# Kernel tuning notes

Hardware: AMD Instinct MI355X
Metric: run time of the kernel (lower is better)

Reference implementation:

```python
import jax, jax.numpy as jnp
import numpy as np

N_CRYST = 64
ATOMS_PER = 32
N = N_CRYST * ATOMS_PER          # 2048 atoms
NBR = 20                         # max_neighbors
E = N * NBR                      # 40960 edges
C = 128                          # sphere_channels(_reduce)
HID = 256                        # hidden_channels
NB = 128                         # num_basis_functions
NLAYER = 8                       # num_interactions
LMAX = 6
K = 1 + 3 * LMAX                 # SH coeffs with mmax=1 -> 19
MAXZ = 100                       # MAX_ATOMIC_NUM
ZDIM = 256
CUT = 8.0
FOUR_PI = 4.0 * np.pi


def sph_harm_m01(d):
    """Real spherical harmonics Y_l^m, l<=LMAX, m in {-1,0,1}. d: [E,3] unit vecs -> [E,K]."""
    x, y, ct = d[:, 0], d[:, 1], d[:, 2]
    rho = jnp.sqrt(x * x + y * y) + 1e-12   # sin(theta)
    cph, sph = x / rho, y / rho
    # Legendre P_l(ct)
    P0 = [jnp.ones_like(ct), ct]
    for l in range(2, LMAX + 1):
        P0.append(((2 * l - 1) * ct * P0[l - 1] - (l - 1) * P0[l - 2]) / l)
    # Associated Legendre P_l^1(ct)
    P1 = {1: -rho, 2: -3.0 * ct * rho}
    for l in range(3, LMAX + 1):
        P1[l] = ((2 * l - 1) * ct * P1[l - 1] - l * P1[l - 2]) / (l - 1)
    Ys = [jnp.full_like(ct, float(np.sqrt(1.0 / FOUR_PI)))]
    for l in range(1, LMAX + 1):
        K0 = float(np.sqrt((2 * l + 1) / FOUR_PI))
        K1 = float(np.sqrt(2.0 * (2 * l + 1) / FOUR_PI / (l * (l + 1))))
        Ys += [K1 * P1[l] * sph, K0 * P0[l], K1 * P1[l] * cph]  # m=-1,0,+1
    return jnp.stack(Ys, axis=-1)


def lattice_from_params(lengths, angles):
    """lengths,angles(deg): [B,3] -> lattice row-vectors [B,3,3]."""
    a, b, c = lengths[:, 0], lengths[:, 1], lengths[:, 2]
    rad = angles * (np.pi / 180.0)
    ca, cb, cg = jnp.cos(rad[:, 0]), jnp.cos(rad[:, 1]), jnp.cos(rad[:, 2])
    sg = jnp.sin(rad[:, 2])
    z0 = jnp.zeros_like(a)
    v3y = (ca - cb * cg) / sg
    v3z = jnp.sqrt(jnp.clip(1.0 - cb * cb - v3y * v3y, 1e-8))
    l1 = jnp.stack([a, z0, z0], -1)
    l2 = jnp.stack([b * cg, b * sg, z0], -1)
    l3 = jnp.stack([c * cb, c * v3y, c * v3z], -1)
    return jnp.stack([l1, l2, l3], axis=1)


def setup_inputs() -> dict:
    key = jax.random.key(0)
    ks = jax.random.split(key, 16)
    z = jax.random.normal(ks[0], (N_CRYST, ZDIM), jnp.float32)
    frac = jax.random.uniform(ks[1], (N, 3), jnp.float32)
    atom_types = jax.random.randint(ks[2], (N,), 1, MAXZ + 1)
    num_atoms = jnp.full((N_CRYST,), ATOMS_PER, jnp.int32)
    lengths = 4.0 + 4.0 * jax.random.uniform(ks[3], (N_CRYST, 3), jnp.float32)
    angles = 80.0 + 20.0 * jax.random.uniform(ks[4], (N_CRYST, 3), jnp.float32)
    batch = jnp.arange(N) // ATOMS_PER
    # NBR incoming edges per atom, sources restricted to the same crystal
    dst = jnp.repeat(jnp.arange(N), NBR)
    src_local = jax.random.randint(ks[5], (E,), 0, ATOMS_PER)
    src = (dst // ATOMS_PER) * ATOMS_PER + src_local
    edge_index = jnp.stack([src, dst], axis=0)
    sc = lambda k, sh, fan: jax.random.normal(k, sh, jnp.float32) / np.sqrt(fan)
    params = dict(
        emb=sc(ks[6], (MAXZ + 1, C), 1.0),
        zproj=sc(ks[7], (ZDIM, C), ZDIM),
        Wd=sc(ks[8], (NLAYER, NB, HID), NB),
        W1=sc(ks[9], (NLAYER, C, HID), C),
        W2=sc(ks[10], (NLAYER, HID, C), HID),
        Wa=sc(ks[11], (C, MAXZ), C),
        ba=jnp.zeros((MAXZ,), jnp.float32),
        wf=sc(ks[12], (C,), C),
    )
    return dict(z=z, pred_frac_coords=frac, pred_atom_types=atom_types,
                num_atoms=num_atoms, lengths=lengths, angles=angles,
                batch=batch, edge_index=edge_index, **params)


def reference(z, pred_frac_coords, pred_atom_types, num_atoms, lengths, angles,
              batch, edge_index, emb, zproj, Wd, W1, W2, Wa, ba, wf):
    lat = lattice_from_params(lengths, angles)                 # [B,3,3]
    pos = jnp.einsum('ni,nij->nj', pred_frac_coords, lat[batch])  # [N,3]
    src, dst = edge_index[0], edge_index[1]
    vec = pos[src] - pos[dst]                                  # [E,3]
    dist = jnp.linalg.norm(vec, axis=-1) + 1e-8
    dirn = vec / dist[:, None]
    offsets = jnp.linspace(0.0, CUT, NB)
    width = offsets[1] - offsets[0]
    rbf = jnp.exp(-0.5 * ((dist[:, None] - offsets) / width) ** 2)  # [E,NB]
    Y = sph_harm_m01(dirn)                                     # [E,K]
    # node SH features, l=0 initialized from atom embedding + latent
    x = jnp.zeros((N, K, C), pred_frac_coords.dtype)
    x = x.at[:, 0, :].set(emb[pred_atom_types] + (z @ zproj)[batch])
    for l in range(NLAYER):
        s = jnp.einsum('ek,ekc->ec', Y, x[src])                # project along edge frame
        h = jax.nn.silu(s @ W1[l] + rbf @ Wd[l])               # [E,HID]
        m = h @ W2[l]                                          # [E,C]
        agg = jax.ops.segment_sum(Y[:, :, None] * m[:, None, :], dst, num_segments=N)
        x = x + agg / NBR
    h_node = x[:, 0, :]                                        # [N,C]
    atom_logits = h_node @ Wa + ba                             # [N,MAXZ]
    fscal = (h_node[src] - h_node[dst]) @ wf                   # [E]
    coord_diff = jax.ops.segment_sum(fscal[:, None] * dirn, dst, num_segments=N)
    return coord_diff, atom_logits
```

## Files before the change

### kernel.cpp

```cpp
#include <hip/hip_runtime.h>
#include <hip/hip_bf16.h>

#define N_CRYST 64
#define ATOMS_PER 32
#define NN 2048
#define NBRS 20
#define EE 40960
#define CC 128
#define HIDDIM 256
#define NBASIS 128
#define NLAYERS 8
#define LMAXV 6
#define KK 19
#define MAXZV 100
#define ZDIMV 256
#define FOUR_PI_F 12.566370614359172f

typedef unsigned short ushort_t;
typedef __attribute__((ext_vector_type(8))) short short8;
typedef __attribute__((ext_vector_type(4))) float floatx4;

__device__ __forceinline__ ushort_t f2us(float f) {
    union { float f; unsigned u; } x;
    x.f = f;
    unsigned r = (x.u + 0x7fffu + ((x.u >> 16) & 1u)) >> 16;
    return (ushort_t)r;
}
__device__ __forceinline__ float us2f(unsigned u) {
    return __uint_as_float(u << 16);
}

__global__ void k_geom(const float* __restrict__ frac, const float* __restrict__ lengths,
                       const float* __restrict__ angles, const int* __restrict__ ei,
                       const float* __restrict__ z, const float* __restrict__ zproj,
                       float* __restrict__ dist, float* __restrict__ dirn,
                       float* __restrict__ Yv, int* __restrict__ trp,
                       int* __restrict__ tloc, float* __restrict__ zc) {
    const int cr = blockIdx.x;
    const int t = threadIdx.x;
    __shared__ float posL[32][3];
    __shared__ int cnt[8][32], base[8][32];

    if (t < 32) {
        int n = cr * 32 + t;
        float la = lengths[cr * 3 + 0];
        float lb = lengths[cr * 3 + 1];
        float lc = lengths[cr * 3 + 2];
        const float D2R = 0.017453292519943295f;
        float aa = angles[cr * 3 + 0] * D2R;
        float ab = angles[cr * 3 + 1] * D2R;
        float ag = angles[cr * 3 + 2] * D2R;
        float ca = cosf(aa), cb = cosf(ab), cg = cosf(ag), sg = sinf(ag);
        float v3y = (ca - cb * cg) / sg;
        float v3z = sqrtf(fmaxf(1.0f - cb * cb - v3y * v3y, 1e-8f));
        float f0 = frac[n * 3 + 0];
        float f1 = frac[n * 3 + 1];
        float f2 = frac[n * 3 + 2];
        posL[t][0] = f0 * la + f1 * (lb * cg) + f2 * (lc * cb);
        posL[t][1] = f1 * (lb * sg) + f2 * (lc * v3y);
        posL[t][2] = f2 * (lc * v3z);
    }
    cnt[t >> 5][t & 31] = 0;
    __syncthreads();

    for (int j = t; j < 640; j += 256) {
        int e = cr * 640 + j;
        int s = ei[e] - cr * 32, d = ei[EE + e] - cr * 32;
        float vx = posL[s][0] - posL[d][0];
        float vy = posL[s][1] - posL[d][1];
        float vz = posL[s][2] - posL[d][2];
        float dd = sqrtf(vx * vx + vy * vy + vz * vz) + 1e-8f;
        float ix = vx / dd, iy = vy / dd, iz = vz / dd;
        dist[e] = dd;
        dirn[e * 3 + 0] = ix;
        dirn[e * 3 + 1] = iy;
        dirn[e * 3 + 2] = iz;

        float ct = iz;
        float rho = sqrtf(ix * ix + iy * iy) + 1e-12f;
        float cph = ix / rho, sph = iy / rho;
        float P0[LMAXV + 1], P1[LMAXV + 1];
        P0[0] = 1.0f;
        P0[1] = ct;
        #pragma unroll
        for (int l = 2; l <= LMAXV; l++)
            P0[l] = ((2 * l - 1) * ct * P0[l - 1] - (l - 1) * P0[l - 2]) / (float)l;
        P1[0] = 0.0f;
        P1[1] = -rho;
        P1[2] = -3.0f * ct * rho;
        #pragma unroll
        for (int l = 3; l <= LMAXV; l++)
            P1[l] = ((2 * l - 1) * ct * P1[l - 1] - l * P1[l - 2]) / (float)(l - 1);

        float* Ye = Yv + (size_t)e * KK;
        Ye[0] = 0.28209479177387814f;
        #pragma unroll
        for (int l = 1; l <= LMAXV; l++) {
            float K0 = sqrtf((2 * l + 1) / FOUR_PI_F);
            float K1 = sqrtf(2.0f * (2 * l + 1) / (FOUR_PI_F * l * (l + 1)));
            Ye[3 * l - 2] = K1 * P1[l] * sph;
            Ye[3 * l - 1] = K0 * P0[l];
            Ye[3 * l]     = K1 * P1[l] * cph;
        }
        atomicAdd(&cnt[j / 80][s], 1);
    }
    __syncthreads();

    if (t < 8) {
        int run = 0;
        for (int a = 0; a < 32; a++) {
            base[t][a] = run;
            trp[(cr * 8 + t) * 33 + a] = run;
            run += cnt[t][a];
        }
        trp[(cr * 8 + t) * 33 + 32] = run;
    }
    __syncthreads();
    cnt[t >> 5][t & 31] = 0;
    __syncthreads();
    for (int j = t; j < 640; j += 256) {
        int e = cr * 640 + j;
        int s = ei[e] - cr * 32;
        int tt = j / 80;
        int slot = base[tt][s] + atomicAdd(&cnt[tt][s], 1);
        tloc[(cr * 8 + tt) * 80 + slot] = j - tt * 80;
    }

    if (t < CC) {
        float acc = 0.f;
        const float* zb = z + (size_t)cr * ZDIMV;
        for (int d = 0; d < ZDIMV; d++) acc += zb[d] * zproj[d * CC + t];
        zc[cr * CC + t] = acc;
    }
}

#define WT_BLKS 3072
#define RBF_BLKS 2560
#define XI_BLKS 4864
__global__ void k_prep(const float* __restrict__ W1, const float* __restrict__ Wd,
                       const float* __restrict__ W2,
                       ushort_t* __restrict__ WT1, ushort_t* __restrict__ WT2,
                       const float* __restrict__ dist, ushort_t* __restrict__ Abf,
                       const int* __restrict__ atype, const int* __restrict__ batch,
                       const float* __restrict__ emb, const float* __restrict__ zc,
                       ushort_t* __restrict__ xbf) {
    const int bid = blockIdx.x;
    const int t = threadIdx.x;
    if (bid < WT_BLKS) {
        int idx = bid * 256 + t;
        const int n1 = NLAYERS * HIDDIM * 256;
        if (idx < n1) {
            int l = idx >> 16;
            int r = idx & 65535;
            int n = r >> 8, k = r & 255;
            float v = (k < 128) ? W1[((size_t)l * CC + k) * HIDDIM + n]
                                : Wd[((size_t)l * NBASIS + (k - 128)) * HIDDIM + n];
            WT1[idx] = f2us(v);
        } else {
            int j = idx - n1;
            int l = j >> 15;
            int r = j & 32767;
            int n = r >> 8, k = r & 255;
            WT2[j] = f2us(W2[((size_t)l * HIDDIM + k) * CC + n]);
        }
    } else if (bid < WT_BLKS + RBF_BLKS) {
        int idx = (bid - WT_BLKS) * 256 + t;
        int e = idx >> 4, j8 = (idx & 15) * 8;
        const float width = 8.0f / 127.0f;
        const float invw = 127.0f / 8.0f;
        float dd = dist[e];
        short8 v;
        #pragma unroll
        for (int jj = 0; jj < 8; jj++) {
            float x = (dd - (float)(j8 + jj) * width) * invw;
            ((ushort_t*)&v)[jj] = f2us(__expf(-0.5f * x * x));
        }
        *(short8*)&Abf[(size_t)e * 256 + 128 + j8] = v;
    } else {
        int idx4 = (bid - WT_BLKS - RBF_BLKS) * 256 + t;
        int basei = idx4 * 4;
        if (basei >= NN * KK * CC) return;
        int n = basei / (KK * CC);
        int r = basei - n * (KK * CC);
        ushort_t v4[4];
        #pragma unroll
        for (int j = 0; j < 4; j++) {
            int rr = r + j;
            float v = 0.f;
            if (rr < CC) v = emb[atype[n] * CC + rr] + zc[batch[n] * CC + rr];
            v4[j] = f2us(v);
        }
        *(uint2*)&xbf[basei] = *(uint2*)v4;
    }
}

__global__ __launch_bounds__(512, 2) void k_layer(const int* __restrict__ trp,
                                                  const int* __restrict__ tloc,
                                                  const float* __restrict__ Yv,
                                                  const ushort_t* __restrict__ Abf,
                                                  const ushort_t* __restrict__ WT1,
                                                  const ushort_t* __restrict__ WT2,
                                                  const ushort_t* __restrict__ xbfin,
                                                  ushort_t* __restrict__ xbfout) {
    __shared__ char smraw[47360];
    ushort_t* As  = (ushort_t*)smraw;
    ushort_t* Hs  = (ushort_t*)smraw;
    ushort_t* Ms  = (ushort_t*)smraw;
    float*   Ylds = (float*)(smraw + 40960);

    const int t = threadIdx.x;
    const int bid = ((blockIdx.x & 7) << 6) | (blockIdx.x >> 3);
    const int w = t >> 6, lane = t & 63;
    const int quad = lane >> 4, lrow = lane & 15;
    const int e0 = bid * 80;
    const int cr = bid >> 3;

    const float* Yb = Yv + (size_t)e0 * KK;
    #pragma unroll
    for (int j = 0; j < 3; j++) {
        int i = t + j * 512;
        if (i < 80 * KK) Ylds[(i / KK) * 20 + (i % KK)] = Yb[i];
    }
    if (t < 80) Ylds[t * 20 + 19] = 0.f;
    __syncthreads();

    short8 arg[3];
    #pragma unroll
    for (int i = 0; i < 3; i++) {
        int idx = i * 512 + t;
        if (idx < 1280) {
            int r = idx >> 4, g16 = idx & 15;
            arg[i] = *(const short8*)(Abf + (size_t)(e0 + r) * 256 + 128 + g16 * 8);
        }
    }

    const int c2 = lane * 2;
    const int sgrp = lane >> 2;
    const int soff = (lane & 3) * 2;
    #pragma unroll 1
    for (int a8 = 0; a8 < 4; a8++) {
        const int a = w * 4 + a8;
        const int i0 = trp[bid * 33 + a];
        const int i1 = trp[bid * 33 + a + 1];
        if (i0 == i1) continue;
        const ushort_t* xsrc = xbfin + (size_t)(cr * 32 + a) * (KK * CC) + c2;
        float2 xr[KK];
        #pragma unroll
        for (int k = 0; k < KK; k++) {
            unsigned u = *(const unsigned*)(xsrc + k * CC);
            xr[k] = make_float2(us2f(u & 0xffffu), us2f(u >> 16));
        }
        for (int i = i0; i < i1; i++) {
            const int r = tloc[bid * 80 + i];
            const float* yp = Ylds + r * 20;
            float ax = 0.f, ay = 0.f;
            #pragma unroll
            for (int k = 0; k < KK; k++) {
                float y = yp[k];
                ax += y * xr[k].x;
                ay += y * xr[k].y;
            }
            unsigned pk = (unsigned)f2us(ax) | (((unsigned)f2us(ay)) << 16);
            *(unsigned*)&As[r * 256 + ((sgrp ^ (r & 7)) << 3) + soff] = pk;
        }
    }

    #pragma unroll
    for (int i = 0; i < 3; i++) {
        int idx = i * 512 + t;
        if (idx < 1280) {
            int r = idx >> 4, g = 16 + (idx & 15);
            *(short8*)&As[r * 256 + ((g ^ (r & 7)) << 3)] = arg[i];
        }
    }

    const ushort_t* W1w = WT1 + (size_t)(w * 32) * 256;
    short8 bp0[2], bp1[2];
    #pragma unroll
    for (int ni = 0; ni < 2; ni++) {
        bp0[ni] = *(const short8*)(W1w + (size_t)(ni * 16 + lrow) * 256 + quad * 8);
        bp1[ni] = *(const short8*)(W1w + (size_t)(ni * 16 + lrow) * 256 + 32 + quad * 8);
    }
    __syncthreads();

    floatx4 acc[5][2];
    #pragma unroll
    for (int mi = 0; mi < 5; mi++)
        #pragma unroll
        for (int ni = 0; ni < 2; ni++) acc[mi][ni] = (floatx4){0.f, 0.f, 0.f, 0.f};

    #pragma unroll
    for (int s8 = 0; s8 < 8; s8++) {
        short8 bcur[2];
        if (s8 & 1) {
            #pragma unroll
            for (int ni = 0; ni < 2; ni++) bcur[ni] = bp1[ni];
            if (s8 < 6) {
                const int kn = (s8 + 2) * 32 + quad * 8;
                #pragma unroll
                for (int ni = 0; ni < 2; ni++)
                    bp1[ni] = *(const short8*)(W1w + (size_t)(ni * 16 + lrow) * 256 + kn);
            }
        } else {
            #pragma unroll
            for (int ni = 0; ni < 2; ni++) bcur[ni] = bp0[ni];
            if (s8 < 6) {
                const int kn = (s8 + 2) * 32 + quad * 8;
                #pragma unroll
                for (int ni = 0; ni < 2; ni++)
                    bp0[ni] = *(const short8*)(W1w + (size_t)(ni * 16 + lrow) * 256 + kn);
            }
        }
        const int grp = s8 * 4 + quad;
        short8 af[5];
        #pragma unroll
        for (int mi = 0; mi < 5; mi++) {
            const int r = mi * 16 + lrow;
            af[mi] = *(const short8*)&As[r * 256 + ((grp ^ (r & 7)) << 3)];
        }
        __builtin_amdgcn_s_setprio(1);
        #pragma unroll
        for (int ni = 0; ni < 2; ni++)
            #pragma unroll
            for (int mi = 0; mi < 5; mi++)
                acc[mi][ni] = __builtin_amdgcn_mfma_f32_16x16x32_bf16(
                    af[mi], bcur[ni], acc[mi][ni], 0, 0, 0);
        __builtin_amdgcn_s_setprio(0);
    }

    const ushort_t* W2w = WT2 + (size_t)(w * 16) * 256;
    short8 bq0, bq1;
    bq0 = *(const short8*)(W2w + (size_t)lrow * 256 + quad * 8);
    bq1 = *(const short8*)(W2w + (size_t)lrow * 256 + 32 + quad * 8);
    __syncthreads();

    #pragma unroll
    for (int mi = 0; mi < 5; mi++) {
        const int row = mi * 16 + quad * 4;
        #pragma unroll
        for (int ni = 0; ni < 2; ni++) {
            const int col = w * 32 + ni * 16 + lrow;
            #pragma unroll
            for (int r = 0; r < 4; r++) {
                float v = acc[mi][ni][r];
                v = v * __builtin_amdgcn_rcpf(1.0f + __expf(-v));
                const int rr = row + r;
                Hs[rr * 256 + ((((col >> 3) ^ (rr & 7)) << 3) | (col & 7))] = f2us(v);
            }
        }
    }
    __syncthreads();

    floatx4 macc[5];
    #pragma unroll
    for (int mi = 0; mi < 5; mi++) macc[mi] = (floatx4){0.f, 0.f, 0.f, 0.f};

    #pragma unroll
    for (int s8 = 0; s8 < 8; s8++) {
        short8 bcur;
        if (s8 & 1) {
            bcur = bq1;
            if (s8 < 6) {
                const int kn = (s8 + 2) * 32 + quad * 8;
                bq1 = *(const short8*)(W2w + (size_t)lrow * 256 + kn);
            }
        } else {
            bcur = bq0;
            if (s8 < 6) {
                const int kn = (s8 + 2) * 32 + quad * 8;
                bq0 = *(const short8*)(W2w + (size_t)lrow * 256 + kn);
            }
        }
        const int grp = s8 * 4 + quad;
        short8 af[5];
        #pragma unroll
        for (int mi = 0; mi < 5; mi++) {
            const int r = mi * 16 + lrow;
            af[mi] = *(const short8*)&Hs[r * 256 + ((grp ^ (r & 7)) << 3)];
        }
        __builtin_amdgcn_s_setprio(1);
        #pragma unroll
        for (int mi = 0; mi < 5; mi++)
            macc[mi] = __builtin_amdgcn_mfma_f32_16x16x32_bf16(
                af[mi], bcur, macc[mi], 0, 0, 0);
        __builtin_amdgcn_s_setprio(0);
    }
    __syncthreads();

    #pragma unroll
    for (int mi = 0; mi < 5; mi++) {
        const int row = mi * 16 + quad * 4;
        const int col = w * 16 + lrow;
        #pragma unroll
        for (int r = 0; r < 4; r++)
            Ms[(row + r) * 132 + col] = f2us(macc[mi][r]);
    }
    __syncthreads();

    const int node = t >> 7;
    const int cq = t & 127;
    const int ng = bid * 4 + node;
    const ushort_t* xbi = xbfin + (size_t)ng * (KK * CC) + cq;
    ushort_t* xbo = xbfout + (size_t)ng * (KK * CC) + cq;

    float xold[KK];
    #pragma unroll
    for (int k = 0; k < KK; k++) xold[k] = us2f((unsigned)xbi[k * CC]);

    float xacc[KK];
    #pragma unroll
    for (int k = 0; k < KK; k++) xacc[k] = 0.f;

    #pragma unroll 4
    for (int e = 0; e < NBRS; e++) {
        const int eg = node * NBRS + e;
        const float m0 = us2f((unsigned)Ms[eg * 132 + cq]);
        const float* yp = Ylds + eg * 20;
        #pragma unroll
        for (int kq = 0; kq < 5; kq++) {
            float4 y = *(const float4*)(yp + kq * 4);
            const int k = kq * 4;
            xacc[k + 0] += y.x * m0;
            xacc[k + 1] += y.y * m0;
            xacc[k + 2] += y.z * m0;
            if (kq < 4) xacc[k + 3] += y.w * m0;
        }
    }
    const float s = 1.0f / (float)NBRS;
    #pragma unroll
    for (int k = 0; k < KK; k++) {
        float nv = xold[k] + xacc[k] * s;
        xbo[k * CC] = f2us(nv);
    }
}

#define COORD_BLKS 512
__global__ void k_head(const int* __restrict__ ei, const ushort_t* __restrict__ xbf,
                       const float* __restrict__ wf, const float* __restrict__ dirn,
                       const float* __restrict__ Wa, const float* __restrict__ ba,
                       float* __restrict__ out) {
    const int bid = blockIdx.x;
    const int t = threadIdx.x;
    if (bid < COORD_BLKS) {
        __shared__ float fs[4][NBRS];
        __shared__ float wsh[CC];
        const int g = t >> 6, lane = t & 63;
        const int n = bid * 4 + g;
        if (t < CC) wsh[t] = wf[t];
        __syncthreads();
        if (lane < NBRS) {
            int e = n * NBRS + lane;
            int sidx = ei[e];
            const ushort_t* xs = xbf + (size_t)sidx * (KK * CC);
            const ushort_t* xd = xbf + (size_t)n * (KK * CC);
            float acc = 0.0f;
            for (int c = 0; c < CC; c++)
                acc += (us2f((unsigned)xs[c]) - us2f((unsigned)xd[c])) * wsh[c];
            fs[g][lane] = acc;
        }
        __syncthreads();
        if (lane < 3) {
            float acc = 0.0f;
            #pragma unroll
            for (int j = 0; j < NBRS; j++)
                acc += fs[g][j] * dirn[(size_t)(n * NBRS + j) * 3 + lane];
            out[n * 3 + lane] = acc;
        }
    } else {
        int idx = (bid - COORD_BLKS) * 256 + t;
        if (idx >= NN * MAXZV) return;
        int n = idx / MAXZV, a = idx - n * MAXZV;
        float acc = ba[a];
        const ushort_t* hn = xbf + (size_t)n * (KK * CC);
        for (int c = 0; c < CC; c++) acc += us2f((unsigned)hn[c]) * Wa[c * MAXZV + a];
        out[NN * 3 + idx] = acc;
    }
}

extern "C" void kernel_launch(void* const* d_in, const int* in_sizes, int n_in,
                              void* d_out, int out_size, void* d_ws, size_t ws_size,
                              hipStream_t stream) {
    (void)in_sizes; (void)n_in; (void)out_size; (void)ws_size;
    const float* z       = (const float*)d_in[0];
    const float* frac    = (const float*)d_in[1];
    const int*   atype   = (const int*)d_in[2];
    const float* lengths = (const float*)d_in[4];
    const float* angles  = (const float*)d_in[5];
    const int*   batch   = (const int*)d_in[6];
    const int*   ei      = (const int*)d_in[7];
    const float* emb     = (const float*)d_in[8];
    const float* zproj   = (const float*)d_in[9];
    const float* Wd      = (const float*)d_in[10];
    const float* W1      = (const float*)d_in[11];
    const float* W2      = (const float*)d_in[12];
    const float* Wa      = (const float*)d_in[13];
    const float* ba      = (const float*)d_in[14];
    const float* wf      = (const float*)d_in[15];
    float* out = (float*)d_out;

    float* ws = (float*)d_ws;
    float* dist = ws; ws += EE;
    float* dirn = ws; ws += EE * 3;
    float* Yv   = ws; ws += (size_t)EE * KK + 4;
    float* zc   = ws; ws += N_CRYST * CC;
    ushort_t* xbfA = (ushort_t*)ws; ws += (size_t)NN * KK * CC / 2;
    ushort_t* xbfB = (ushort_t*)ws; ws += (size_t)NN * KK * CC / 2;
    int* trp  = (int*)ws;
    int* tloc = trp + 512 * 33;
    ushort_t* Abf  = (ushort_t*)(tloc + 512 * 80);
    ushort_t* WT1  = Abf + (size_t)EE * 256;
    ushort_t* WT2  = WT1 + (size_t)NLAYERS * 256 * 256;

    k_geom<<<N_CRYST, 256, 0, stream>>>(frac, lengths, angles, ei, z, zproj,
                                        dist, dirn, Yv, trp, tloc, zc);
    k_prep<<<WT_BLKS + RBF_BLKS + XI_BLKS, 256, 0, stream>>>(W1, Wd, W2, WT1, WT2,
                                                             dist, Abf, atype, batch,
                                                             emb, zc, xbfA);

    for (int l = 0; l < NLAYERS; l++) {
        const ushort_t* xbi = (l & 1) ? xbfB : xbfA;
        ushort_t*       xbo = (l & 1) ? xbfA : xbfB;
        k_layer<<<512, 512, 0, stream>>>(trp, tloc, Yv, Abf,
                                         WT1 + (size_t)l * 256 * 256,
                                         WT2 + (size_t)l * CC * HIDDIM,
                                         xbi, xbo);
    }

    k_head<<<COORD_BLKS + (NN * MAXZV) / 256, 256, 0, stream>>>(ei, xbfA, wf, dirn,
                                                                Wa, ba, out);
}
```

Before: 411.5 us.

## Fuse next-layer edge projection into layer epilogue and compact RBF buffer

After each layer updates the node features, the same threads now project the fresh node state onto the outgoing edges of that node (via a new per-crystal CSR of source edges) and write the next layer's edge input s in bf16. The following layer then loads s directly into shared memory instead of gathering 19xC node features per edge and reducing them. The RBF buffer is also shrunk to 128 columns per edge. This trades the gather-and-reduce prologue for extra global traffic: scattered Y reads from global memory and an additional E×C bf16 write and read per layer.

```diff
diff --git a/kernel.cpp b/kernel.cpp
--- a/kernel.cpp
+++ b/kernel.cpp
@@ -35,11 +35,13 @@
                        const float* __restrict__ z, const float* __restrict__ zproj,
                        float* __restrict__ dist, float* __restrict__ dirn,
                        float* __restrict__ Yv, int* __restrict__ trp,
-                       int* __restrict__ tloc, float* __restrict__ zc) {
+                       int* __restrict__ tloc, int* __restrict__ crow,
+                       int* __restrict__ corig, float* __restrict__ zc) {
     const int cr = blockIdx.x;
     const int t = threadIdx.x;
     __shared__ float posL[32][3];
     __shared__ int cnt[8][32], base[8][32];
+    __shared__ int ccnt[32], cbs[32];
 
     if (t < 32) {
         int n = cr * 32 + t;
@@ -59,6 +61,7 @@
         posL[t][0] = f0 * la + f1 * (lb * cg) + f2 * (lc * cb);
         posL[t][1] = f1 * (lb * sg) + f2 * (lc * v3y);
         posL[t][2] = f2 * (lc * v3z);
+        ccnt[t] = 0;
     }
     cnt[t >> 5][t & 31] = 0;
     __syncthreads();
@@ -103,6 +106,7 @@
             Ye[3 * l]     = K1 * P1[l] * cph;
         }
         atomicAdd(&cnt[j / 80][s], 1);
+        atomicAdd(&ccnt[s], 1);
     }
     __syncthreads();
 
@@ -115,8 +119,18 @@
         }
         trp[(cr * 8 + t) * 33 + 32] = run;
     }
+    if (t == 8) {
+        int run = 0;
+        for (int a = 0; a < 32; a++) {
+            cbs[a] = run;
+            crow[cr * 33 + a] = run;
+            run += ccnt[a];
+        }
+        crow[cr * 33 + 32] = run;
+    }
     __syncthreads();
     cnt[t >> 5][t & 31] = 0;
+    if (t < 32) ccnt[t] = 0;
     __syncthreads();
     for (int j = t; j < 640; j += 256) {
         int e = cr * 640 + j;
@@ -124,6 +138,8 @@
         int tt = j / 80;
         int slot = base[tt][s] + atomicAdd(&cnt[tt][s], 1);
         tloc[(cr * 8 + tt) * 80 + slot] = j - tt * 80;
+        int slot2 = cbs[s] + atomicAdd(&ccnt[s], 1);
+        corig[cr * 640 + slot2] = e;
     }
 
     if (t < CC) {
@@ -175,7 +191,7 @@
             float x = (dd - (float)(j8 + jj) * width) * invw;
             ((ushort_t*)&v)[jj] = f2us(__expf(-0.5f * x * x));
         }
-        *(short8*)&Abf[(size_t)e * 256 + 128 + j8] = v;
+        *(short8*)&Abf[(size_t)e * 128 + j8] = v;
     } else {
         int idx4 = (bid - WT_BLKS - RBF_BLKS) * 256 + t;
         int basei = idx4 * 4;
@@ -196,12 +212,17 @@
 
 __global__ __launch_bounds__(512, 2) void k_layer(const int* __restrict__ trp,
                                                   const int* __restrict__ tloc,
+                                                  const int* __restrict__ crow,
+                                                  const int* __restrict__ corig,
                                                   const float* __restrict__ Yv,
                                                   const ushort_t* __restrict__ Abf,
                                                   const ushort_t* __restrict__ WT1,
                                                   const ushort_t* __restrict__ WT2,
                                                   const ushort_t* __restrict__ xbfin,
-                                                  ushort_t* __restrict__ xbfout) {
+                                                  ushort_t* __restrict__ xbfout,
+                                                  const ushort_t* __restrict__ sIn,
+                                                  ushort_t* __restrict__ sOut,
+                                                  int first, int last) {
     __shared__ char smraw[47360];
     ushort_t* As  = (ushort_t*)smraw;
     ushort_t* Hs  = (ushort_t*)smraw;
@@ -230,38 +251,50 @@
         int idx = i * 512 + t;
         if (idx < 1280) {
             int r = idx >> 4, g16 = idx & 15;
-            arg[i] = *(const short8*)(Abf + (size_t)(e0 + r) * 256 + 128 + g16 * 8);
-        }
-    }
-
-    const int c2 = lane * 2;
-    const int sgrp = lane >> 2;
-    const int soff = (lane & 3) * 2;
-    #pragma unroll 1
-    for (int a8 = 0; a8 < 4; a8++) {
-        const int a = w * 4 + a8;
-        const int i0 = trp[bid * 33 + a];
-        const int i1 = trp[bid * 33 + a + 1];
-        if (i0 == i1) continue;
-        const ushort_t* xsrc = xbfin + (size_t)(cr * 32 + a) * (KK * CC) + c2;
-        float2 xr[KK];
-        #pragma unroll
-        for (int k = 0; k < KK; k++) {
-            unsigned u = *(const unsigned*)(xsrc + k * CC);
-            xr[k] = make_float2(us2f(u & 0xffffu), us2f(u >> 16));
-        }
-        for (int i = i0; i < i1; i++) {
-            const int r = tloc[bid * 80 + i];
-            const float* yp = Ylds + r * 20;
-            float ax = 0.f, ay = 0.f;
+            arg[i] = *(const short8*)(Abf + (size_t)(e0 + r) * 128 + g16 * 8);
+        }
+    }
+
+    if (first) {
+        const int c2 = lane * 2;
+        const int sgrp = lane >> 2;
+        const int soff = (lane & 3) * 2;
+        #pragma unroll 1
+        for (int a8 = 0; a8 < 4; a8++) {
+            const int a = w * 4 + a8;
+            const int i0 = trp[bid * 33 + a];
+            const int i1 = trp[bid * 33 + a + 1];
+            if (i0 == i1) continue;
+            const ushort_t* xsrc = xbfin + (size_t)(cr * 32 + a) * (KK * CC) + c2;
+            float2 xr[KK];
             #pragma unroll
             for (int k = 0; k < KK; k++) {
-                float y = yp[k];
-                ax += y * xr[k].x;
-                ay += y * xr[k].y;
-            }
-            unsigned pk = (unsigned)f2us(ax) | (((unsigned)f2us(ay)) << 16);
-            *(unsigned*)&As[r * 256 + ((sgrp ^ (r & 7)) << 3) + soff] = pk;
+                unsigned u = *(const unsigned*)(xsrc + k * CC);
+                xr[k] = make_float2(us2f(u & 0xffffu), us2f(u >> 16));
+            }
+            for (int i = i0; i < i1; i++) {
+                const int r = tloc[bid * 80 + i];
+                const float* yp = Ylds + r * 20;
+                float ax = 0.f, ay = 0.f;
+                #pragma unroll
+                for (int k = 0; k < KK; k++) {
+                    float y = yp[k];
+                    ax += y * xr[k].x;
+                    ay += y * xr[k].y;
+                }
+                unsigned pk = (unsigned)f2us(ax) | (((unsigned)f2us(ay)) << 16);
+                *(unsigned*)&As[r * 256 + ((sgrp ^ (r & 7)) << 3) + soff] = pk;
+            }
+        }
+    } else {
+        #pragma unroll
+        for (int i = 0; i < 3; i++) {
+            int idx = i * 512 + t;
+            if (idx < 1280) {
+                int r = idx >> 4, g16 = idx & 15;
+                short8 v = *(const short8*)(sIn + (size_t)(e0 + r) * 128 + g16 * 8);
+                *(short8*)&As[r * 256 + ((g16 ^ (r & 7)) << 3)] = v;
+            }
         }
     }
 
@@ -403,10 +436,6 @@
     const ushort_t* xbi = xbfin + (size_t)ng * (KK * CC) + cq;
     ushort_t* xbo = xbfout + (size_t)ng * (KK * CC) + cq;
 
-    float xold[KK];
-    #pragma unroll
-    for (int k = 0; k < KK; k++) xold[k] = us2f((unsigned)xbi[k * CC]);
-
     float xacc[KK];
     #pragma unroll
     for (int k = 0; k < KK; k++) xacc[k] = 0.f;
@@ -429,8 +458,23 @@
     const float s = 1.0f / (float)NBRS;
     #pragma unroll
     for (int k = 0; k < KK; k++) {
-        float nv = xold[k] + xacc[k] * s;
+        float nv = us2f((unsigned)xbi[k * CC]) + xacc[k] * s;
+        xacc[k] = nv;
         xbo[k * CC] = f2us(nv);
+    }
+
+    if (!last) {
+        const int a = ng & 31;
+        const int i0c = crow[cr * 33 + a];
+        const int i1c = crow[cr * 33 + a + 1];
+        for (int i = i0c; i < i1c; i++) {
+            const int e = corig[cr * 640 + i];
+            const float* yp = Yv + (size_t)e * KK;
+            float acc2 = 0.f;
+            #pragma unroll
+            for (int k = 0; k < KK; k++) acc2 += yp[k] * xacc[k];
+            sOut[(size_t)e * 128 + cq] = f2us(acc2);
+        }
     }
 }
 
@@ -505,14 +549,18 @@
     float* zc   = ws; ws += N_CRYST * CC;
     ushort_t* xbfA = (ushort_t*)ws; ws += (size_t)NN * KK * CC / 2;
     ushort_t* xbfB = (ushort_t*)ws; ws += (size_t)NN * KK * CC / 2;
-    int* trp  = (int*)ws;
-    int* tloc = trp + 512 * 33;
-    ushort_t* Abf  = (ushort_t*)(tloc + 512 * 80);
-    ushort_t* WT1  = Abf + (size_t)EE * 256;
+    ushort_t* sA   = (ushort_t*)ws; ws += (size_t)EE * 128 / 2;
+    ushort_t* sB   = (ushort_t*)ws; ws += (size_t)EE * 128 / 2;
+    int* trp   = (int*)ws;
+    int* tloc  = trp + 512 * 33;
+    int* crow  = tloc + 512 * 80;
+    int* corig = crow + 64 * 33 + 3;
+    ushort_t* Abf  = (ushort_t*)(corig + EE);
+    ushort_t* WT1  = Abf + (size_t)EE * 128;
     ushort_t* WT2  = WT1 + (size_t)NLAYERS * 256 * 256;
 
     k_geom<<<N_CRYST, 256, 0, stream>>>(frac, lengths, angles, ei, z, zproj,
-                                        dist, dirn, Yv, trp, tloc, zc);
+                                        dist, dirn, Yv, trp, tloc, crow, corig, zc);
     k_prep<<<WT_BLKS + RBF_BLKS + XI_BLKS, 256, 0, stream>>>(W1, Wd, W2, WT1, WT2,
                                                              dist, Abf, atype, batch,
                                                              emb, zc, xbfA);
@@ -520,10 +568,13 @@
     for (int l = 0; l < NLAYERS; l++) {
         const ushort_t* xbi = (l & 1) ? xbfB : xbfA;
         ushort_t*       xbo = (l & 1) ? xbfA : xbfB;
-        k_layer<<<512, 512, 0, stream>>>(trp, tloc, Yv, Abf,
+        const ushort_t* sin = (l & 1) ? sB : sA;
+        ushort_t*       sou = (l & 1) ? sA : sB;
+        k_layer<<<512, 512, 0, stream>>>(trp, tloc, crow, corig, Yv, Abf,
                                          WT1 + (size_t)l * 256 * 256,
                                          WT2 + (size_t)l * CC * HIDDIM,
-                                         xbi, xbo);
+                                         xbi, xbo, sin, sou,
+                                         (l == 0) ? 1 : 0, (l == NLAYERS - 1) ? 1 : 0);
     }
 
     k_head<<<COORD_BLKS + (NN * MAXZV) / 256, 256, 0, stream>>>(ei, xbfA, wf, dirn,
```

Result: slower. 485.5 us (+18.0%).
